# Kernel optimization log

Hardware: AMD Instinct MI355X
Metric: run time of the kernel (lower is better)

## Reference

```python
import jax, jax.numpy as jnp
import numpy as np

EMB = 512
HEADS = 16
WH, WW = 8, 8
N = WH * WW
B = 2048
CPB_HID = 512
EPS = 1e-12


def _buffers():
    # continuous relative coords table, shape (1, 2*WH-1, 2*WW-1, 2)
    ch = np.arange(-(WH - 1), WH, dtype=np.float32)
    cw = np.arange(-(WW - 1), WW, dtype=np.float32)
    t = np.stack(np.meshgrid(ch, cw, indexing='ij')).transpose(1, 2, 0)[None].copy()
    t[..., 0] /= (WH - 1)
    t[..., 1] /= (WW - 1)
    t *= 8.0
    t = np.sign(t) * np.log2(np.abs(t) + 1.0) / np.log2(8.0)
    # relative position index, shape (N, N), values in [0, (2*WH-1)*(2*WW-1))
    coords = np.stack(np.meshgrid(np.arange(WH), np.arange(WW), indexing='ij'))
    cf = coords.reshape(2, -1)
    rel = (cf[:, :, None] - cf[:, None, :]).transpose(1, 2, 0).copy()
    rel[..., 0] += WH - 1
    rel[..., 1] += WW - 1
    rel[..., 0] *= 2 * WW - 1
    idx = rel.sum(-1)
    return jnp.asarray(t, jnp.float32), jnp.asarray(idx, jnp.int32)


def setup_inputs() -> dict:
    key = jax.random.key(0)
    ks = jax.random.split(key, 8)
    rel_table, rel_index = _buffers()
    s = 0.02
    return {
        'x': jax.random.normal(ks[0], (B, N, EMB), jnp.float32),
        'qkv_w': jax.random.normal(ks[1], (3 * EMB, EMB), jnp.float32) * s,
        'q_bias': jnp.zeros((EMB,), jnp.float32),
        'v_bias': jnp.zeros((EMB,), jnp.float32),
        'flex_attn': jnp.full((HEADS, 1, 1), np.log(10.0), jnp.float32),
        'cpb_w1': jax.random.normal(ks[2], (CPB_HID, 2), jnp.float32) * s,
        'cpb_b1': jnp.zeros((CPB_HID,), jnp.float32),
        'cpb_w2': jax.random.normal(ks[3], (HEADS, CPB_HID), jnp.float32) * s,
        'proj_w': jax.random.normal(ks[4], (EMB, EMB), jnp.float32) * s,
        'proj_b': jnp.zeros((EMB,), jnp.float32),
        'rel_table': rel_table,
        'rel_index': rel_index,
    }


def reference(x, qkv_w, q_bias, v_bias, flex_attn, cpb_w1, cpb_b1, cpb_w2,
              proj_w, proj_b, rel_table, rel_index):
    Bx, Nx, C = x.shape
    H = HEADS
    D = C // H
    # qkv with bias only on q and v (k bias is zero), as in the torch code
    qkv_bias = jnp.concatenate([q_bias, jnp.zeros_like(v_bias), v_bias])
    qkv = x @ qkv_w.T + qkv_bias                      # (B, N, 3C)
    qkv = qkv.reshape(Bx, Nx, 3, H, D).transpose(2, 0, 3, 1, 4)
    q, k, v = qkv[0], qkv[1], qkv[2]                  # each (B, H, N, D)
    # cosine attention: L2-normalize q and k
    qn = q / jnp.maximum(jnp.linalg.norm(q, axis=-1, keepdims=True), EPS)
    kn = k / jnp.maximum(jnp.linalg.norm(k, axis=-1, keepdims=True), EPS)
    attn = jnp.einsum('bhnd,bhmd->bhnm', qn, kn)      # (B, H, N, N)
    # learned per-head temperature, clamped at 1/0.01
    scale = jnp.exp(jnp.minimum(flex_attn, jnp.log(jnp.float32(100.0))))  # (H,1,1)
    attn = attn * scale[None]
    # continuous relative position bias via MLP + gather
    bias_tab = jax.nn.relu(rel_table @ cpb_w1.T + cpb_b1) @ cpb_w2.T      # (1, 2WH-1, 2WW-1, H)
    bias_tab = bias_tab.reshape(-1, H)
    bias = bias_tab[rel_index.reshape(-1)].reshape(Nx, Nx, H)
    bias = 16.0 * jax.nn.sigmoid(bias.transpose(2, 0, 1))                 # (H, N, N)
    attn = jax.nn.softmax(attn + bias[None], axis=-1)
    out = jnp.einsum('bhnm,bhmd->bhnd', attn, v)      # (B, H, N, D)
    out = out.transpose(0, 2, 1, 3).reshape(Bx, Nx, C)
    return out @ proj_w.T + proj_b
```

## Files before the change

kernel.cpp:

```cpp
#include <hip/hip_runtime.h>

using bf16x8 = __attribute__((ext_vector_type(8))) short;
using f32x4  = __attribute__((ext_vector_type(4))) float;
using f32x16 = __attribute__((ext_vector_type(16))) float;

static constexpr int EMB = 512, HEADS = 16, NTOK = 64, BWIN = 2048;
static constexpr int MROWS = BWIN * NTOK;
static constexpr int QKVN  = 3 * EMB;

__device__ __forceinline__ float bf2f(unsigned int u) {
  union { unsigned int i; float f; } c; c.i = u << 16; return c.f;
}
__device__ __forceinline__ unsigned short f2bf(float x) {
  union { float f; unsigned int i; } c; c.f = x;
  return (unsigned short)((c.i + 0x7fffu + ((c.i >> 16) & 1u)) >> 16);
}
__device__ __forceinline__ void gload_lds16(const void* g, void* l) {
  __builtin_amdgcn_global_load_lds((const __attribute__((address_space(1))) void*)g,
                                   (__attribute__((address_space(3))) void*)l, 16, 0, 0);
}
__device__ __forceinline__ unsigned int cvt_pk_bf16(float lo, float hi) {
  unsigned int d;
  asm("v_cvt_pk_bf16_f32 %0, %1, %2" : "=v"(d) : "v"(lo), "v"(hi));
  return d;
}

#define BARRIER() __builtin_amdgcn_s_barrier()
#define LGKM0()  do { asm volatile("s_waitcnt lgkmcnt(0)" ::: "memory"); \
                      __builtin_amdgcn_sched_barrier(0); } while (0)
#define VMCNT2() do { asm volatile("s_waitcnt vmcnt(2)" ::: "memory"); \
                      __builtin_amdgcn_sched_barrier(0); } while (0)

__global__ __launch_bounds__(256) void xcast(const float* __restrict__ x,
                                             unsigned short* __restrict__ xb) {
  size_t i = ((size_t)blockIdx.x * 256 + threadIdx.x) * 8;
  float4 a = *(const float4*)(x + i);
  float4 b = *(const float4*)(x + i + 4);
  ushort4 lo = make_ushort4(f2bf(a.x), f2bf(a.y), f2bf(a.z), f2bf(a.w));
  ushort4 hi = make_ushort4(f2bf(b.x), f2bf(b.y), f2bf(b.z), f2bf(b.w));
  *(ushort4*)(xb + i) = lo;
  *(ushort4*)(xb + i + 4) = hi;
}

__global__ void prep_weights(const float* __restrict__ qkv_w, const float* __restrict__ proj_w,
                             const float* __restrict__ q_bias, const float* __restrict__ v_bias,
                             unsigned short* __restrict__ wq, unsigned short* __restrict__ wp,
                             float* __restrict__ qkv_bias) {
  int i = blockIdx.x * 256 + threadIdx.x;
  wq[i] = f2bf(qkv_w[i]);
  if (i < EMB * EMB) wp[i] = f2bf(proj_w[i]);
  if (i < EMB) {
    qkv_bias[i]           = q_bias[i];
    qkv_bias[EMB + i]     = 0.f;
    qkv_bias[2 * EMB + i] = v_bias[i];
  }
}

__global__ __launch_bounds__(64) void cpb_mlp(const float* __restrict__ tbl,
                        const float* __restrict__ w1, const float* __restrict__ b1,
                        const float* __restrict__ w2, float* __restrict__ tab) {
  __shared__ float hid[512];
  const int p = blockIdx.x, t = threadIdx.x;
  const float t0 = tbl[p * 2], t1 = tbl[p * 2 + 1];
  #pragma unroll
  for (int s = 0; s < 8; ++s) {
    int j = t + s * 64;
    hid[j] = fmaxf(0.f, t0 * w1[j * 2] + t1 * w1[j * 2 + 1] + b1[j]);
  }
  __syncthreads();
  const int h = t >> 2, q = t & 3;
  float sum = 0.f;
  for (int j = q * 128; j < q * 128 + 128; ++j) sum += hid[j] * w2[h * 512 + j];
  sum += __shfl_xor(sum, 1);
  sum += __shfl_xor(sum, 2);
  if (q == 0) tab[p * 16 + h] = sum;
}

__global__ void cpb_expand(const float* __restrict__ tab, const int* __restrict__ rel_index,
                           float* __restrict__ biasT) {
  int e = blockIdx.x * 256 + threadIdx.x;
  int h = e >> 12, ij = e & 4095;
  int kk = ij >> 6, q = ij & 63;
  float x = tab[rel_index[q * 64 + kk] * 16 + h];
  biasT[e] = 16.f / (1.f + __expf(-x));
}

template<bool OUT_F32, int NBX, int KT>
__global__ __launch_bounds__(512, 2) void gemm256(const unsigned short* __restrict__ Ap,
    const unsigned short* __restrict__ Bp, const float* __restrict__ bias,
    void* __restrict__ Cp, int M, int N) {
  __shared__ unsigned short As[2][256 * 64];
  __shared__ unsigned short Bs[2][256 * 64];
  constexpr int NT = KT / 64;
  constexpr int NITER = NT / 2;
  const int t = threadIdx.x;
  const int l = t & 63, w = t >> 6;
  const int lr = l & 15, lg = l >> 4;
  const int q8 = gridDim.x >> 3;
  const int wgid = (blockIdx.x & 7) * q8 + (blockIdx.x >> 3);
  const int n0 = (wgid % NBX) * 256, m0 = (wgid / NBX) * 256;
  const int wm = (w >> 2) * 128, wn = (w & 3) * 64;
  const int ha128 = (w >> 2) * 128;
  const int srow = t >> 3;
  const int scol = ((t & 7) ^ (srow & 7)) << 3;
  const unsigned short* Abase = Ap + (size_t)m0 * KT;
  const unsigned short* Bbase = Bp + (size_t)n0 * KT;

  f32x4 acc[8][4];
  #pragma unroll
  for (int i = 0; i < 8; ++i)
    #pragma unroll
    for (int j = 0; j < 4; ++j) acc[i][j] = (f32x4){0.f, 0.f, 0.f, 0.f};
  bf16x8 afr[4][2], bfr[4][2];

  auto stage_half = [&](int d, int kt, int half, bool isA) {
    const unsigned short* g = (isA ? Abase : Bbase)
        + (size_t)(half * 128 + srow) * KT + kt * 64 + scol;
    unsigned short* lds = (isA ? &As[d][0] : &Bs[d][0]) + half * 8192 + (t >> 6) * 512;
    gload_lds16(g, lds);
    gload_lds16(g + (size_t)64 * KT, lds + 4096);
  };
  auto ldA4 = [&](int d, int mb) {
    #pragma unroll
    for (int m = 0; m < 4; ++m) {
      int row = ha128 + (mb + m) * 16 + lr;
      #pragma unroll
      for (int ks = 0; ks < 2; ++ks)
        afr[m][ks] = *(const bf16x8*)(&As[d][row * 64 + ((((ks << 2) + lg) ^ (lr & 7)) << 3)]);
    }
  };
  auto ldB2 = [&](int d, int nb) {
    #pragma unroll
    for (int n = 0; n < 2; ++n) {
      int row = wn + (nb + n) * 16 + lr;
      #pragma unroll
      for (int ks = 0; ks < 2; ++ks)
        bfr[nb + n][ks] = *(const bf16x8*)(&Bs[d][row * 64 + ((((ks << 2) + lg) ^ (lr & 7)) << 3)]);
    }
  };
  auto mfmaQ = [&](int mb, int nb) {
    __builtin_amdgcn_s_setprio(1);
    #pragma unroll
    for (int ks = 0; ks < 2; ++ks)
      #pragma unroll
      for (int m = 0; m < 4; ++m)
        #pragma unroll
        for (int n = 0; n < 2; ++n)
          acc[mb + m][nb + n] = __builtin_amdgcn_mfma_f32_16x16x32_bf16(
              afr[m][ks], bfr[nb + n][ks], acc[mb + m][nb + n], 0, 0, 0);
    __builtin_amdgcn_s_setprio(0);
  };

  stage_half(0, 0, 0, true);  stage_half(0, 0, 1, true);
  stage_half(0, 0, 0, false); stage_half(0, 0, 1, false);
  stage_half(1, (NT > 1 ? 1 : 0), 0, true);
  VMCNT2();
  BARRIER();

  for (int i = 0; i < NITER; ++i) {
    const int kt1 = 2 * i + 1;
    const int kt2 = (2 * i + 2 < NT) ? 2 * i + 2 : NT - 1;
    const int kt3 = (2 * i + 3 < NT) ? 2 * i + 3 : NT - 1;
    ldA4(0, 0); ldB2(0, 0);
    stage_half(1, kt1, 1, true);
    BARRIER(); LGKM0(); mfmaQ(0, 0); BARRIER();
    ldB2(0, 2);
    stage_half(1, kt1, 0, false);
    BARRIER(); LGKM0(); mfmaQ(0, 2); BARRIER();
    ldA4(0, 4);
    stage_half(1, kt1, 1, false);
    BARRIER(); LGKM0(); mfmaQ(4, 2); BARRIER();
    stage_half(0, kt2, 0, true);
    VMCNT2(); BARRIER(); mfmaQ(4, 0); BARRIER();
    ldA4(1, 0); ldB2(1, 0);
    stage_half(0, kt2, 1, true);
    BARRIER(); LGKM0(); mfmaQ(0, 0); BARRIER();
    ldB2(1, 2);
    stage_half(0, kt2, 0, false);
    BARRIER(); LGKM0(); mfmaQ(0, 2); BARRIER();
    ldA4(1, 4);
    stage_half(0, kt2, 1, false);
    BARRIER(); LGKM0(); mfmaQ(4, 2); BARRIER();
    stage_half(1, kt3, 0, true);
    VMCNT2(); BARRIER(); mfmaQ(4, 0); BARRIER();
  }

  #pragma unroll
  for (int mf = 0; mf < 8; ++mf)
    #pragma unroll
    for (int nf = 0; nf < 4; ++nf)
      #pragma unroll
      for (int r = 0; r < 4; ++r) {
        int mm = m0 + wm + mf * 16 + lg * 4 + r;
        int nn = n0 + wn + nf * 16 + lr;
        float v = acc[mf][nf][r] + bias[nn];
        if (OUT_F32) ((float*)Cp)[(size_t)mm * N + nn] = v;
        else ((unsigned short*)Cp)[(size_t)mm * N + nn] = f2bf(v);
      }
}

__global__ __launch_bounds__(256, 3) void attn_win4(const unsigned short* __restrict__ qkv,
    const float* __restrict__ biasT, const float* __restrict__ flex,
    unsigned short* __restrict__ aout) {
  __shared__ __align__(16) unsigned short kq[16384];
  __shared__ __align__(16) unsigned short vTall[4][2048];
  const int t = threadIdx.x;
  const int l = t & 63, w = t >> 6;
  const int lq = l & 31, hi = l >> 5;
  const int g = (blockIdx.x & 7) * (gridDim.x >> 3) + (blockIdx.x >> 3);
  const int b = g >> 2;
  const int p = g & 3;
  const int h = p * 4 + w;
  const unsigned short* base = qkv + (size_t)b * NTOK * QKVN;
  const float scale = __expf(fminf(flex[h], 4.6051701860f));

  const uint4* vp = (const uint4*)(base + (size_t)l * QKVN + 2 * EMB + h * 32);
  uint4 v0 = vp[0], v1 = vp[1], v2 = vp[2], v3 = vp[3];

  #pragma unroll
  for (int i = 0; i < 8; ++i) {
    int sl  = (w * 8 + i) * 64 + l;
    int tok = sl >> 5, sec = (sl >> 4) & 1, phys = sl & 15;
    int log = phys ^ (tok & 15);
    gload_lds16(base + (size_t)tok * QKVN + (sec ? EMB : 0) + p * 128 + log * 8,
                kq + (size_t)(w * 8 + i) * 512);
  }

  unsigned short* vT = vTall[w];
  {
    unsigned int wd[16] = {v0.x, v0.y, v0.z, v0.w, v1.x, v1.y, v1.z, v1.w,
                           v2.x, v2.y, v2.z, v2.w, v3.x, v3.y, v3.z, v3.w};
    #pragma unroll
    for (int d = 0; d < 32; ++d) {
      unsigned short val = (d & 1) ? (unsigned short)(wd[d >> 1] >> 16)
                                   : (unsigned short)(wd[d >> 1] & 0xffffu);
      vT[d * 64 + (((l >> 3) ^ (d & 7)) << 3) + (l & 7)] = val;
    }
  }
  __syncthreads();

  bf16x8 kfr[2][2], qfr[2][2];
  #pragma unroll
  for (int f = 0; f < 2; ++f) {
    #pragma unroll
    for (int which = 0; which < 2; ++which) {
      const int tok = f * 32 + lq;
      const int sec = which ? 0 : 1;
      const unsigned short* row = kq + tok * 256 + sec * 128;
      const int ls0 = w * 4 + hi;
      const int ls1 = w * 4 + 2 + hi;
      uint4 r0 = *(const uint4*)(row + ((ls0 ^ (tok & 15)) << 3));
      uint4 r1 = *(const uint4*)(row + ((ls1 ^ (tok & 15)) << 3));
      unsigned int wd[8] = {r0.x, r0.y, r0.z, r0.w, r1.x, r1.y, r1.z, r1.w};
      float fv[16];
      #pragma unroll
      for (int e = 0; e < 8; ++e) {
        fv[2 * e]     = bf2f(wd[e] & 0xffffu);
        fv[2 * e + 1] = bf2f(wd[e] >> 16);
      }
      float ss = 0.f;
      #pragma unroll
      for (int e = 0; e < 16; ++e) ss += fv[e] * fv[e];
      ss += __shfl_xor(ss, 32);
      float inv = (which ? scale : 1.f) / fmaxf(sqrtf(ss), 1e-12f);
      bf16x8 f0, f1;
      #pragma unroll
      for (int e = 0; e < 8; ++e) {
        f0[e] = (short)f2bf(fv[e] * inv);
        f1[e] = (short)f2bf(fv[8 + e] * inv);
      }
      if (which) { qfr[f][0] = f0; qfr[f][1] = f1; }
      else       { kfr[f][0] = f0; kfr[f][1] = f1; }
    }
  }

  bf16x8 bv[4];
  #pragma unroll
  for (int c = 0; c < 4; ++c)
    bv[c] = *(const bf16x8*)(&vT[lq * 64 + ((((2 * c + hi) ^ (lq & 7))) << 3)]);

  const f32x16 z16 = (f32x16)(0.f);

  #pragma unroll
  for (int qf = 0; qf < 2; ++qf) {
    f32x16 s0 = __builtin_amdgcn_mfma_f32_32x32x16_bf16(kfr[0][0], qfr[qf][0], z16, 0, 0, 0);
    s0 = __builtin_amdgcn_mfma_f32_32x32x16_bf16(kfr[0][1], qfr[qf][1], s0, 0, 0, 0);
    f32x16 s1 = __builtin_amdgcn_mfma_f32_32x32x16_bf16(kfr[1][0], qfr[qf][0], z16, 0, 0, 0);
    s1 = __builtin_amdgcn_mfma_f32_32x32x16_bf16(kfr[1][1], qfr[qf][1], s1, 0, 0, 0);

    float p2[32];
    const float* bt = biasT + (size_t)h * 4096 + qf * 32 + lq;
    #pragma unroll
    for (int r = 0; r < 16; ++r) {
      int kkb = (r & 3) + 8 * (r >> 2) + 4 * hi;
      p2[r]      = s0[r] + bt[kkb * 64];
      p2[16 + r] = s1[r] + bt[(32 + kkb) * 64];
    }
    float mx = p2[0];
    #pragma unroll
    for (int e = 1; e < 32; ++e) mx = fmaxf(mx, p2[e]);
    mx = fmaxf(mx, __shfl_xor(mx, 32));
    float sum = 0.f;
    #pragma unroll
    for (int e = 0; e < 32; ++e) { p2[e] = __expf(p2[e] - mx); sum += p2[e]; }
    sum += __shfl_xor(sum, 32);
    const float inv = 1.f / sum;
    #pragma unroll
    for (int e = 0; e < 32; ++e) p2[e] *= inv;

    unsigned int wp_[2][8], sw[2][8];
    #pragma unroll
    for (int kf = 0; kf < 2; ++kf)
      #pragma unroll
      for (int m = 0; m < 8; ++m) {
        wp_[kf][m] = cvt_pk_bf16(p2[kf * 16 + 2 * m], p2[kf * 16 + 2 * m + 1]);
        sw[kf][m]  = (unsigned int)__builtin_amdgcn_ds_bpermute(
                        ((l ^ 32) & 63) << 2, (int)wp_[kf][m]);
      }
    f32x16 oacc = z16;
    #pragma unroll
    for (int c = 0; c < 4; ++c) {
      const int kf = c >> 1, mlo = (c & 1) * 4;
      unsigned int d0 = hi ? sw[kf][mlo + 2] : wp_[kf][mlo + 0];
      unsigned int d1 = hi ? sw[kf][mlo + 3] : wp_[kf][mlo + 1];
      unsigned int d2 = hi ? wp_[kf][mlo + 2] : sw[kf][mlo + 0];
      unsigned int d3 = hi ? wp_[kf][mlo + 3] : sw[kf][mlo + 1];
      union { uint4 u; bf16x8 v; } pa;
      pa.u = make_uint4(d0, d1, d2, d3);
      oacc = __builtin_amdgcn_mfma_f32_32x32x16_bf16(pa.v, bv[c], oacc, 0, 0, 0);
    }
    #pragma unroll
    for (int r = 0; r < 16; ++r) {
      int q = qf * 32 + (r & 3) + 8 * (r >> 2) + 4 * hi;
      aout[(size_t)(b * NTOK + q) * EMB + h * 32 + lq] = f2bf(oacc[r]);
    }
  }
}

extern "C" void kernel_launch(void* const* d_in, const int* in_sizes, int n_in,
                              void* d_out, int out_size, void* d_ws, size_t ws_size,
                              hipStream_t stream) {
  const float* x         = (const float*)d_in[0];
  const float* qkv_w     = (const float*)d_in[1];
  const float* q_bias    = (const float*)d_in[2];
  const float* v_bias    = (const float*)d_in[3];
  const float* flex      = (const float*)d_in[4];
  const float* cpb_w1    = (const float*)d_in[5];
  const float* cpb_b1    = (const float*)d_in[6];
  const float* cpb_w2    = (const float*)d_in[7];
  const float* proj_w    = (const float*)d_in[8];
  const float* proj_b    = (const float*)d_in[9];
  const float* rel_table = (const float*)d_in[10];
  const int*   rel_index = (const int*)d_in[11];

  char* ws = (char*)d_ws;
  unsigned short* qkv_bf = (unsigned short*)(ws + 0);
  unsigned short* xb     = (unsigned short*)(ws + 402653184ull);
  unsigned short* ao_bf  = (unsigned short*)(ws + 402653184ull);
  unsigned short* wq_bf  = (unsigned short*)(ws + 536870912ull);
  unsigned short* wp_bf  = (unsigned short*)(ws + 538443776ull);
  float* qkv_bias        = (float*)(ws + 538968064ull);
  float* tab             = (float*)(ws + 538974208ull);
  float* biasT           = (float*)(ws + 538988608ull);

  xcast<<<32768, 256, 0, stream>>>(x, xb);
  prep_weights<<<3072, 256, 0, stream>>>(qkv_w, proj_w, q_bias, v_bias, wq_bf, wp_bf, qkv_bias);
  cpb_mlp<<<225, 64, 0, stream>>>(rel_table, cpb_w1, cpb_b1, cpb_w2, tab);
  cpb_expand<<<256, 256, 0, stream>>>(tab, rel_index, biasT);
  gemm256<false, 6, EMB><<<3072, 512, 0, stream>>>(
      xb, wq_bf, qkv_bias, (void*)qkv_bf, MROWS, QKVN);
  attn_win4<<<BWIN * 4, 256, 0, stream>>>(qkv_bf, biasT, flex, ao_bf);
  gemm256<true, 2, EMB><<<1024, 512, 0, stream>>>(
      ao_bf, wp_bf, proj_b, d_out, MROWS, EMB);
}
```

Baseline: 632.2 us.

## Reuse K/Q LDS for V transpose, use analytic softmax max, raise occupancy

The attention kernel now writes the transposed V tile into the K/Q shared buffer once the normalized fragments are in registers, dropping the separate 16 KB V buffer and adding a barrier. This lowers LDS use so launch bounds can ask for four blocks per SIMD instead of three. Softmax uses a fixed upper bound (scale+16) as the max instead of a per-row max reduction, which holds because cosine scores are bounded and the bias is in [0,16]. The lane-swap bpermutes move into the PV loop to shorten register live ranges.

```diff
diff --git a/kernel.cpp b/kernel.cpp
--- a/kernel.cpp
+++ b/kernel.cpp
@@ -199,11 +199,10 @@
       }
 }
 
-__global__ __launch_bounds__(256, 3) void attn_win4(const unsigned short* __restrict__ qkv,
+__global__ __launch_bounds__(256, 4) void attn_win6(const unsigned short* __restrict__ qkv,
     const float* __restrict__ biasT, const float* __restrict__ flex,
     unsigned short* __restrict__ aout) {
   __shared__ __align__(16) unsigned short kq[16384];
-  __shared__ __align__(16) unsigned short vTall[4][2048];
   const int t = threadIdx.x;
   const int l = t & 63, w = t >> 6;
   const int lq = l & 31, hi = l >> 5;
@@ -224,18 +223,6 @@
     int log = phys ^ (tok & 15);
     gload_lds16(base + (size_t)tok * QKVN + (sec ? EMB : 0) + p * 128 + log * 8,
                 kq + (size_t)(w * 8 + i) * 512);
-  }
-
-  unsigned short* vT = vTall[w];
-  {
-    unsigned int wd[16] = {v0.x, v0.y, v0.z, v0.w, v1.x, v1.y, v1.z, v1.w,
-                           v2.x, v2.y, v2.z, v2.w, v3.x, v3.y, v3.z, v3.w};
-    #pragma unroll
-    for (int d = 0; d < 32; ++d) {
-      unsigned short val = (d & 1) ? (unsigned short)(wd[d >> 1] >> 16)
-                                   : (unsigned short)(wd[d >> 1] & 0xffffu);
-      vT[d * 64 + (((l >> 3) ^ (d & 7)) << 3) + (l & 7)] = val;
-    }
   }
   __syncthreads();
 
@@ -273,6 +260,20 @@
       else       { kfr[f][0] = f0; kfr[f][1] = f1; }
     }
   }
+  __syncthreads();
+
+  unsigned short* vT = kq + w * 2048;
+  {
+    unsigned int wd[16] = {v0.x, v0.y, v0.z, v0.w, v1.x, v1.y, v1.z, v1.w,
+                           v2.x, v2.y, v2.z, v2.w, v3.x, v3.y, v3.z, v3.w};
+    #pragma unroll
+    for (int d = 0; d < 32; ++d) {
+      unsigned short val = (d & 1) ? (unsigned short)(wd[d >> 1] >> 16)
+                                   : (unsigned short)(wd[d >> 1] & 0xffffu);
+      vT[d * 64 + (((l >> 3) ^ (d & 7)) << 3) + (l & 7)] = val;
+    }
+  }
+  asm volatile("" ::: "memory");
 
   bf16x8 bv[4];
   #pragma unroll
@@ -280,6 +281,7 @@
     bv[c] = *(const bf16x8*)(&vT[lq * 64 + ((((2 * c + hi) ^ (lq & 7))) << 3)]);
 
   const f32x16 z16 = (f32x16)(0.f);
+  const float mx = scale + 16.0f;
 
   #pragma unroll
   for (int qf = 0; qf < 2; ++qf) {
@@ -288,43 +290,42 @@
     f32x16 s1 = __builtin_amdgcn_mfma_f32_32x32x16_bf16(kfr[1][0], qfr[qf][0], z16, 0, 0, 0);
     s1 = __builtin_amdgcn_mfma_f32_32x32x16_bf16(kfr[1][1], qfr[qf][1], s1, 0, 0, 0);
 
-    float p2[32];
+    float e_[32];
     const float* bt = biasT + (size_t)h * 4096 + qf * 32 + lq;
+    float sum = 0.f;
     #pragma unroll
     for (int r = 0; r < 16; ++r) {
       int kkb = (r & 3) + 8 * (r >> 2) + 4 * hi;
-      p2[r]      = s0[r] + bt[kkb * 64];
-      p2[16 + r] = s1[r] + bt[(32 + kkb) * 64];
-    }
-    float mx = p2[0];
-    #pragma unroll
-    for (int e = 1; e < 32; ++e) mx = fmaxf(mx, p2[e]);
-    mx = fmaxf(mx, __shfl_xor(mx, 32));
-    float sum = 0.f;
-    #pragma unroll
-    for (int e = 0; e < 32; ++e) { p2[e] = __expf(p2[e] - mx); sum += p2[e]; }
+      e_[r]      = __expf(s0[r] + bt[kkb * 64] - mx);
+      e_[16 + r] = __expf(s1[r] + bt[(32 + kkb) * 64] - mx);
+      sum += e_[r] + e_[16 + r];
+    }
     sum += __shfl_xor(sum, 32);
     const float inv = 1.f / sum;
-    #pragma unroll
-    for (int e = 0; e < 32; ++e) p2[e] *= inv;
-
-    unsigned int wp_[2][8], sw[2][8];
+
+    unsigned int wp_[2][8];
     #pragma unroll
     for (int kf = 0; kf < 2; ++kf)
       #pragma unroll
-      for (int m = 0; m < 8; ++m) {
-        wp_[kf][m] = cvt_pk_bf16(p2[kf * 16 + 2 * m], p2[kf * 16 + 2 * m + 1]);
-        sw[kf][m]  = (unsigned int)__builtin_amdgcn_ds_bpermute(
-                        ((l ^ 32) & 63) << 2, (int)wp_[kf][m]);
-      }
+      for (int m = 0; m < 8; ++m)
+        wp_[kf][m] = cvt_pk_bf16(e_[kf * 16 + 2 * m] * inv, e_[kf * 16 + 2 * m + 1] * inv);
+
     f32x16 oacc = z16;
     #pragma unroll
     for (int c = 0; c < 4; ++c) {
       const int kf = c >> 1, mlo = (c & 1) * 4;
-      unsigned int d0 = hi ? sw[kf][mlo + 2] : wp_[kf][mlo + 0];
-      unsigned int d1 = hi ? sw[kf][mlo + 3] : wp_[kf][mlo + 1];
-      unsigned int d2 = hi ? wp_[kf][mlo + 2] : sw[kf][mlo + 0];
-      unsigned int d3 = hi ? wp_[kf][mlo + 3] : sw[kf][mlo + 1];
+      unsigned int sw0 = (unsigned int)__builtin_amdgcn_ds_bpermute(
+                            ((l ^ 32) & 63) << 2, (int)wp_[kf][mlo + 0]);
+      unsigned int sw1 = (unsigned int)__builtin_amdgcn_ds_bpermute(
+                            ((l ^ 32) & 63) << 2, (int)wp_[kf][mlo + 1]);
+      unsigned int sw2 = (unsigned int)__builtin_amdgcn_ds_bpermute(
+                            ((l ^ 32) & 63) << 2, (int)wp_[kf][mlo + 2]);
+      unsigned int sw3 = (unsigned int)__builtin_amdgcn_ds_bpermute(
+                            ((l ^ 32) & 63) << 2, (int)wp_[kf][mlo + 3]);
+      unsigned int d0 = hi ? sw2 : wp_[kf][mlo + 0];
+      unsigned int d1 = hi ? sw3 : wp_[kf][mlo + 1];
+      unsigned int d2 = hi ? wp_[kf][mlo + 2] : sw0;
+      unsigned int d3 = hi ? wp_[kf][mlo + 3] : sw1;
       union { uint4 u; bf16x8 v; } pa;
       pa.u = make_uint4(d0, d1, d2, d3);
       oacc = __builtin_amdgcn_mfma_f32_32x32x16_bf16(pa.v, bv[c], oacc, 0, 0, 0);
@@ -369,7 +370,7 @@
   cpb_expand<<<256, 256, 0, stream>>>(tab, rel_index, biasT);
   gemm256<false, 6, EMB><<<3072, 512, 0, stream>>>(
       xb, wq_bf, qkv_bias, (void*)qkv_bf, MROWS, QKVN);
-  attn_win4<<<BWIN * 4, 256, 0, stream>>>(qkv_bf, biasT, flex, ao_bf);
+  attn_win6<<<BWIN * 4, 256, 0, stream>>>(qkv_bf, biasT, flex, ao_bf);
   gemm256<true, 2, EMB><<<1024, 512, 0, stream>>>(
       ao_bf, wp_bf, proj_b, d_out, MROWS, EMB);
 }
```

After: 654.0 us. 1.03x slower.
